# Performance work log

Measured on AMD Instinct MI355X. Metric: run time of the kernel, lower is better.

The kernel has to match this reference:

```python
import jax, jax.numpy as jnp
import numpy as np

NUM_CLASSES = 80


def _bce_logits(x, y):
    # numerically stable BCEWithLogits, elementwise
    return jnp.maximum(x, 0.0) - x * y + jnp.log1p(jnp.exp(-jnp.abs(x)))


def _iou_center(b1, b2):
    # boxes in (cx, cy, w, h) format, last dim = 4; returns IoU, last dim dropped
    b1x1 = b1[..., 0] - b1[..., 2] / 2
    b1y1 = b1[..., 1] - b1[..., 3] / 2
    b1x2 = b1[..., 0] + b1[..., 2] / 2
    b1y2 = b1[..., 1] + b1[..., 3] / 2
    b2x1 = b2[..., 0] - b2[..., 2] / 2
    b2y1 = b2[..., 1] - b2[..., 3] / 2
    b2x2 = b2[..., 0] + b2[..., 2] / 2
    b2y2 = b2[..., 1] + b2[..., 3] / 2
    iw = jnp.clip(jnp.minimum(b1x2, b2x2) - jnp.maximum(b1x1, b2x1), 0.0)
    ih = jnp.clip(jnp.minimum(b1y2, b2y2) - jnp.maximum(b1y1, b2y1), 0.0)
    inter = iw * ih
    union = (b1x2 - b1x1) * (b1y2 - b1y1) + (b2x2 - b2x1) * (b2y2 - b2y1) - inter
    return inter / (union + 1e-16)


def setup_inputs() -> dict:
    key = jax.random.key(0)
    kp, ko, kxy, kwh, kc, ka = jax.random.split(key, 6)
    B, A, S = 32, 3, 52
    predictions = jax.random.normal(kp, (B, A, S, S, 5 + NUM_CLASSES), dtype=jnp.float32)
    obj_flag = jax.random.bernoulli(ko, 0.3, (B, A, S, S, 1)).astype(jnp.float32)
    xy = jax.random.uniform(kxy, (B, A, S, S, 2), dtype=jnp.float32)
    wh = jax.random.uniform(kwh, (B, A, S, S, 2), minval=0.05, maxval=1.5, dtype=jnp.float32)
    cls = jax.random.randint(kc, (B, A, S, S, 1), 0, NUM_CLASSES).astype(jnp.float32)
    target = jnp.concatenate([obj_flag, xy, wh, cls], axis=-1)
    anchors = jax.random.uniform(ka, (3, 2), minval=0.1, maxval=1.0, dtype=jnp.float32)
    return {"predictions": predictions, "target": target, "anchors": anchors}


def reference(predictions, target, anchors):
    obj = (target[..., 0] == 1).astype(predictions.dtype)    # [B,3,S,S]
    noobj = (target[..., 0] == 0).astype(predictions.dtype)  # [B,3,S,S]
    n_obj = jnp.sum(obj)
    n_noobj = jnp.sum(noobj)

    anchors_r = anchors.reshape(1, 3, 1, 1, 2)
    pred_obj = predictions[..., 0]
    tgt_obj = target[..., 0]

    # noobj BCE (masked mean over noobj cells)
    no_detection = jnp.sum(_bce_logits(pred_obj, tgt_obj) * noobj) / n_noobj

    # decoded boxes and IoU (detached)
    pred_xy = jax.nn.sigmoid(predictions[..., 1:3])
    pred_wh_dec = jnp.exp(predictions[..., 3:5]) * anchors_r
    box_preds = jnp.concatenate([pred_xy, pred_wh_dec], axis=-1)
    ious = jax.lax.stop_gradient(_iou_center(box_preds, target[..., 1:5]))  # [B,3,S,S]

    # obj BCE against IoU-scaled targets (masked mean over obj cells)
    detection = jnp.sum(_bce_logits(pred_obj, ious * tgt_obj) * obj) / n_obj

    # box MSE: sigmoid(xy) & raw wh vs target xy & log(wh/anchors)
    pred_box = jnp.concatenate([pred_xy, predictions[..., 3:5]], axis=-1)
    tgt_box = jnp.concatenate(
        [target[..., 1:3], jnp.log(1e-16 + target[..., 3:5] / anchors_r)], axis=-1)
    box = jnp.sum(((pred_box - tgt_box) ** 2) * obj[..., None]) / (4.0 * n_obj)

    # classification CE (masked mean over obj cells)
    logp = jax.nn.log_softmax(predictions[..., 5:], axis=-1)
    labels = target[..., 5].astype(jnp.int32)
    nll = -jnp.take_along_axis(logp, labels[..., None], axis=-1)[..., 0]
    classification = jnp.sum(nll * obj) / n_obj

    return box + detection + no_detection + classification
```

## Files before the change

### kernel.cpp

```cpp
#include <hip/hip_runtime.h>

#define NTHREADS  256
#define STRIDE    85
#define SSPAN     2704
#define NEG_HUGE  -3.0e38f

__device__ __forceinline__ float wave_reduce(float v) {
    #pragma unroll
    for (int off = 32; off > 0; off >>= 1)
        v += __shfl_down(v, off, 64);
    return v;
}

__global__ __launch_bounds__(NTHREADS) void loss_partial(
    const float* __restrict__ pred, const float* __restrict__ tgt,
    const float* __restrict__ anchors, float* __restrict__ partial,
    int n_cells, int ngroups)
{
    __shared__ float red[4][6];

    const int tid  = threadIdx.x;
    const int lane = tid & 63;
    const int wid  = tid >> 6;

    const float aw0 = anchors[0], ah0 = anchors[1];
    const float aw1 = anchors[2], ah1 = anchors[3];
    const float aw2 = anchors[4], ah2 = anchors[5];

    float a_obj = 0.f, a_nobj = 0.f, a_bceo = 0.f, a_bceno = 0.f,
          a_box = 0.f, a_cls = 0.f;

    const int gstride = gridDim.x * 4;
    for (int g = blockIdx.x * 4 + wid; g < ngroups; g += gstride) {
        const int cbase = g * 64;
        const int cell  = cbase + lane;
        const bool valid = cell < n_cells;

        float t0 = -1.f, t1 = 0.f, t2 = 0.f, t3 = 0.f, t4 = 0.f, t5 = 0.f;
        float p0 = 0.f;
        if (valid) {
            const float* tc = tgt + (size_t)cell * 6;
            t0 = tc[0]; t1 = tc[1]; t2 = tc[2];
            t3 = tc[3]; t4 = tc[4]; t5 = tc[5];
            p0 = pred[(size_t)cell * STRIDE];
        }
        const float bce_base = fmaxf(p0, 0.f) + log1pf(__expf(-fabsf(p0)));
        if (t0 == 0.0f) { a_nobj += 1.f; a_bceno += bce_base; }
        if (t0 == 1.0f) { a_obj  += 1.f; }

        unsigned long long m = __ballot(t0 == 1.0f);

        int c0 = -1; float f1a = 0.f, f2a = 0.f;
        if (m) {
            c0 = __ffsll(m) - 1; m &= m - 1;
            const float* b = pred + (size_t)(cbase + c0) * STRIDE;
            f1a = b[1 + lane];
            if (lane < 20) f2a = b[65 + lane];
        }
        while (c0 >= 0) {
            int c1 = -1; float f1b = 0.f, f2b = 0.f;
            if (m) {
                c1 = __ffsll(m) - 1; m &= m - 1;
                const float* b = pred + (size_t)(cbase + c1) * STRIDE;
                f1b = b[1 + lane];
                if (lane < 20) f2b = b[65 + lane];
            }
            {
                const int cg = cbase + c0;
                const float m1 = (lane >= 4) ? f1a : NEG_HUGE;
                const float m2 = (lane < 20) ? f2a : NEG_HUGE;
                float mx = fmaxf(m1, m2);
                #pragma unroll
                for (int o = 32; o; o >>= 1) mx = fmaxf(mx, __shfl_xor(mx, o, 64));
                float e = ((lane >= 4) ? __expf(f1a - mx) : 0.f)
                        + ((lane < 20) ? __expf(f2a - mx) : 0.f);
                #pragma unroll
                for (int o = 32; o; o >>= 1) e += __shfl_xor(e, o, 64);

                const float tb1 = __shfl(t1, c0, 64), tb2 = __shfl(t2, c0, 64);
                const float tb3 = __shfl(t3, c0, 64), tb4 = __shfl(t4, c0, 64);
                const float tb5 = __shfl(t5, c0, 64);
                const float pb0 = __shfl(p0, c0, 64);
                const float bb  = __shfl(bce_base, c0, 64);
                const float pp1 = __shfl(f1a, 0, 64), pp2 = __shfl(f1a, 1, 64);
                const float pp3 = __shfl(f1a, 2, 64), pp4 = __shfl(f1a, 3, 64);

                const int   label = (int)tb5;
                const int   idx   = 5 + label;
                const float s1 = __shfl(f1a, (idx - 1) & 63, 64);
                const float s2 = __shfl(f2a, (idx - 65) & 63, 64);
                const float lv = (idx <= 64) ? s1 : s2;

                const int aidx = (cg / SSPAN) % 3;
                const float aw = aidx == 0 ? aw0 : (aidx == 1 ? aw1 : aw2);
                const float ah = aidx == 0 ? ah0 : (aidx == 1 ? ah1 : ah2);

                const float sx = 1.f / (1.f + __expf(-pp1));
                const float sy = 1.f / (1.f + __expf(-pp2));
                const float pw = __expf(pp3) * aw, ph = __expf(pp4) * ah;
                const float b1x1 = sx - pw * 0.5f, b1x2 = sx + pw * 0.5f;
                const float b1y1 = sy - ph * 0.5f, b1y2 = sy + ph * 0.5f;
                const float b2x1 = tb1 - tb3 * 0.5f, b2x2 = tb1 + tb3 * 0.5f;
                const float b2y1 = tb2 - tb4 * 0.5f, b2y2 = tb2 + tb4 * 0.5f;
                const float iw = fmaxf(fminf(b1x2, b2x2) - fmaxf(b1x1, b2x1), 0.f);
                const float ih = fmaxf(fminf(b1y2, b2y2) - fmaxf(b1y1, b2y1), 0.f);
                const float inter = iw * ih;
                const float uni = (b1x2 - b1x1) * (b1y2 - b1y1)
                                + (b2x2 - b2x1) * (b2y2 - b2y1) - inter;
                const float iou = inter / (uni + 1e-16f);

                const float vbceo = bb - pb0 * iou;
                const float lw = logf(1e-16f + tb3 / aw);
                const float lh = logf(1e-16f + tb4 / ah);
                const float d0 = sx - tb1, d1 = sy - tb2;
                const float d2 = pp3 - lw, d3 = pp4 - lh;
                const float vbox = d0 * d0 + d1 * d1 + d2 * d2 + d3 * d3;
                const float vcls = (mx + __logf(e)) - lv;

                if (lane == c0) {
                    a_bceo += vbceo;
                    a_box  += vbox;
                    a_cls  += vcls;
                }
            }
            c0 = c1; f1a = f1b; f2a = f2b;
        }
    }

    float vals[6] = {a_obj, a_nobj, a_bceo, a_bceno, a_box, a_cls};
    #pragma unroll
    for (int k = 0; k < 6; ++k) {
        const float r = wave_reduce(vals[k]);
        if (lane == 0) red[wid][k] = r;
    }
    __syncthreads();
    if (tid == 0) {
        #pragma unroll
        for (int k = 0; k < 6; ++k)
            partial[blockIdx.x * 6 + k] =
                red[0][k] + red[1][k] + red[2][k] + red[3][k];
    }
}

__global__ __launch_bounds__(NTHREADS) void loss_final(
    const float* __restrict__ partial, int nblocks, float* __restrict__ out)
{
    __shared__ float red[4][6];
    const int tid = threadIdx.x, lane = tid & 63, wid = tid >> 6;
    float s[6] = {0.f, 0.f, 0.f, 0.f, 0.f, 0.f};
    for (int i = tid; i < nblocks; i += NTHREADS) {
        #pragma unroll
        for (int k = 0; k < 6; ++k) s[k] += partial[i * 6 + k];
    }
    #pragma unroll
    for (int k = 0; k < 6; ++k) {
        const float r = wave_reduce(s[k]);
        if (lane == 0) red[wid][k] = r;
    }
    __syncthreads();
    if (tid == 0) {
        float t[6];
        #pragma unroll
        for (int k = 0; k < 6; ++k)
            t[k] = red[0][k] + red[1][k] + red[2][k] + red[3][k];
        const float n_obj = t[0], n_noobj = t[1];
        out[0] = t[2] / n_obj + t[3] / n_noobj
               + t[4] / (4.f * n_obj) + t[5] / n_obj;
    }
}

extern "C" void kernel_launch(void* const* d_in, const int* in_sizes, int n_in,
                              void* d_out, int out_size, void* d_ws, size_t ws_size,
                              hipStream_t stream) {
    const float* pred    = (const float*)d_in[0];
    const float* tgt     = (const float*)d_in[1];
    const float* anchors = (const float*)d_in[2];
    float* out = (float*)d_out;

    const int n_cells = in_sizes[1] / 6;
    const int ngroups = (n_cells + 63) / 64;
    int grid = (ngroups + 3) / 4;
    if (grid > 2048) grid = 2048;
    if (grid < 1)    grid = 1;
    float* partial = (float*)d_ws;

    loss_partial<<<grid, NTHREADS, 0, stream>>>(pred, tgt, anchors, partial,
                                                n_cells, ngroups);
    loss_final<<<1, NTHREADS, 0, stream>>>(partial, grid, out);
}
```

Baseline: 163.9 us.

## Compact object cells into shared queue and process four lanes per cell

Replaces the per-wave serial loop over object cells, where a whole 64-lane wave handled one cell at a time with wide shuffles, with a block-level compaction. Object cells in a 256-cell tile are written to a shared-memory queue, and each cell is then handled by 4 lanes that load 20 class logits apiece and reduce with 4-wide shuffles. The aim is to use far more of each wave per object cell and to drop the serial dependency chain. In exchange it adds __syncthreads barriers per tile and contiguous per-lane loads that are less coalesced. Target loads also switch to float2.

After: 135.9 us. 1.21x faster.

```diff
diff --git a/kernel.cpp b/kernel.cpp
--- a/kernel.cpp
+++ b/kernel.cpp
@@ -1,9 +1,10 @@
 #include <hip/hip_runtime.h>
 
 #define NTHREADS  256
+#define TILE      256
 #define STRIDE    85
 #define SSPAN     2704
-#define NEG_HUGE  -3.0e38f
+#define MAXGRID   2048
 
 __device__ __forceinline__ float wave_reduce(float v) {
     #pragma unroll
@@ -15,13 +16,19 @@
 __global__ __launch_bounds__(NTHREADS) void loss_partial(
     const float* __restrict__ pred, const float* __restrict__ tgt,
     const float* __restrict__ anchors, float* __restrict__ partial,
-    int n_cells, int ngroups)
+    int n_cells, int n_tiles)
 {
+    __shared__ int   qcell[TILE];
+    __shared__ int   qlab [TILE];
+    __shared__ float qt1[TILE], qt2[TILE], qt3[TILE], qt4[TILE];
+    __shared__ float qp0[TILE], qbb[TILE];
+    __shared__ int   wcnt[4];
     __shared__ float red[4][6];
 
     const int tid  = threadIdx.x;
     const int lane = tid & 63;
     const int wid  = tid >> 6;
+    const int part = tid & 3;
 
     const float aw0 = anchors[0], ah0 = anchors[1];
     const float aw1 = anchors[2], ah1 = anchors[3];
@@ -30,68 +37,74 @@
     float a_obj = 0.f, a_nobj = 0.f, a_bceo = 0.f, a_bceno = 0.f,
           a_box = 0.f, a_cls = 0.f;
 
-    const int gstride = gridDim.x * 4;
-    for (int g = blockIdx.x * 4 + wid; g < ngroups; g += gstride) {
-        const int cbase = g * 64;
-        const int cell  = cbase + lane;
+    for (int tile = blockIdx.x; tile < n_tiles; tile += gridDim.x) {
+        const int cell  = tile * TILE + tid;
         const bool valid = cell < n_cells;
 
         float t0 = -1.f, t1 = 0.f, t2 = 0.f, t3 = 0.f, t4 = 0.f, t5 = 0.f;
         float p0 = 0.f;
         if (valid) {
-            const float* tc = tgt + (size_t)cell * 6;
-            t0 = tc[0]; t1 = tc[1]; t2 = tc[2];
-            t3 = tc[3]; t4 = tc[4]; t5 = tc[5];
+            const float2* tc2 = (const float2*)(tgt + (size_t)cell * 6);
+            const float2 a = tc2[0], b = tc2[1], c = tc2[2];
+            t0 = a.x; t1 = a.y; t2 = b.x; t3 = b.y; t4 = c.x; t5 = c.y;
             p0 = pred[(size_t)cell * STRIDE];
         }
         const float bce_base = fmaxf(p0, 0.f) + log1pf(__expf(-fabsf(p0)));
         if (t0 == 0.0f) { a_nobj += 1.f; a_bceno += bce_base; }
-        if (t0 == 1.0f) { a_obj  += 1.f; }
+        const bool isobj = (t0 == 1.0f);
+        if (isobj) a_obj += 1.f;
 
-        unsigned long long m = __ballot(t0 == 1.0f);
+        const unsigned long long m = __ballot(isobj);
+        if (lane == 0) wcnt[wid] = __popcll(m);
+        __syncthreads();
+        int off = 0;
+        #pragma unroll
+        for (int w = 0; w < 4; ++w) if (w < wid) off += wcnt[w];
+        const int nq = wcnt[0] + wcnt[1] + wcnt[2] + wcnt[3];
+        if (isobj) {
+            const int rank = off + __popcll(m & ((1ull << lane) - 1ull));
+            qcell[rank] = cell;
+            qt1[rank] = t1; qt2[rank] = t2; qt3[rank] = t3; qt4[rank] = t4;
+            qlab[rank] = (int)t5;
+            qp0[rank]  = p0;
+            qbb[rank]  = bce_base;
+        }
+        __syncthreads();
 
-        int c0 = -1; float f1a = 0.f, f2a = 0.f;
-        if (m) {
-            c0 = __ffsll(m) - 1; m &= m - 1;
-            const float* b = pred + (size_t)(cbase + c0) * STRIDE;
-            f1a = b[1 + lane];
-            if (lane < 20) f2a = b[65 + lane];
-        }
-        while (c0 >= 0) {
-            int c1 = -1; float f1b = 0.f, f2b = 0.f;
-            if (m) {
-                c1 = __ffsll(m) - 1; m &= m - 1;
-                const float* b = pred + (size_t)(cbase + c1) * STRIDE;
-                f1b = b[1 + lane];
-                if (lane < 20) f2b = b[65 + lane];
-            }
-            {
-                const int cg = cbase + c0;
-                const float m1 = (lane >= 4) ? f1a : NEG_HUGE;
-                const float m2 = (lane < 20) ? f2a : NEG_HUGE;
-                float mx = fmaxf(m1, m2);
-                #pragma unroll
-                for (int o = 32; o; o >>= 1) mx = fmaxf(mx, __shfl_xor(mx, o, 64));
-                float e = ((lane >= 4) ? __expf(f1a - mx) : 0.f)
-                        + ((lane < 20) ? __expf(f2a - mx) : 0.f);
-                #pragma unroll
-                for (int o = 32; o; o >>= 1) e += __shfl_xor(e, o, 64);
+        const int nr = (nq + 63) >> 6;
+        for (int r = 0; r < nr; ++r) {
+            const int qi  = r * 64 + (tid >> 2);
+            const bool act = qi < nq;
+            const int cellg = act ? qcell[qi] : 0;
+            const float* pc = pred + (size_t)cellg * STRIDE;
 
-                const float tb1 = __shfl(t1, c0, 64), tb2 = __shfl(t2, c0, 64);
-                const float tb3 = __shfl(t3, c0, 64), tb4 = __shfl(t4, c0, 64);
-                const float tb5 = __shfl(t5, c0, 64);
-                const float pb0 = __shfl(p0, c0, 64);
-                const float bb  = __shfl(bce_base, c0, 64);
-                const float pp1 = __shfl(f1a, 0, 64), pp2 = __shfl(f1a, 1, 64);
-                const float pp3 = __shfl(f1a, 2, 64), pp4 = __shfl(f1a, 3, 64);
+            float v[20];
+            const float* cp = pc + 5 + part * 20;
+            #pragma unroll
+            for (int k = 0; k < 20; ++k) v[k] = cp[k];
+            float mx = v[0];
+            #pragma unroll
+            for (int k = 1; k < 20; ++k) mx = fmaxf(mx, v[k]);
+            mx = fmaxf(mx, __shfl_xor(mx, 1, 4));
+            mx = fmaxf(mx, __shfl_xor(mx, 2, 4));
+            float se = 0.f;
+            #pragma unroll
+            for (int k = 0; k < 20; ++k) se += __expf(v[k] - mx);
+            se += __shfl_xor(se, 1, 4);
+            se += __shfl_xor(se, 2, 4);
 
-                const int   label = (int)tb5;
-                const int   idx   = 5 + label;
-                const float s1 = __shfl(f1a, (idx - 1) & 63, 64);
-                const float s2 = __shfl(f2a, (idx - 65) & 63, 64);
-                const float lv = (idx <= 64) ? s1 : s2;
+            const float pp  = pc[1 + part];
+            const float pp1 = __shfl(pp, 0, 4), pp2 = __shfl(pp, 1, 4);
+            const float pp3 = __shfl(pp, 2, 4), pp4 = __shfl(pp, 3, 4);
 
-                const int aidx = (cg / SSPAN) % 3;
+            if (part == 0 && act) {
+                const float tb1 = qt1[qi], tb2 = qt2[qi];
+                const float tb3 = qt3[qi], tb4 = qt4[qi];
+                const int   label = qlab[qi];
+                const float pb0 = qp0[qi], bb = qbb[qi];
+                const float lv  = pc[5 + label];
+
+                const int aidx = (cellg / SSPAN) % 3;
                 const float aw = aidx == 0 ? aw0 : (aidx == 1 ? aw1 : aw2);
                 const float ah = aidx == 0 ? ah0 : (aidx == 1 ? ah1 : ah2);
 
@@ -109,22 +122,16 @@
                                 + (b2x2 - b2x1) * (b2y2 - b2y1) - inter;
                 const float iou = inter / (uni + 1e-16f);
 
-                const float vbceo = bb - pb0 * iou;
+                a_bceo += bb - pb0 * iou;
                 const float lw = logf(1e-16f + tb3 / aw);
                 const float lh = logf(1e-16f + tb4 / ah);
                 const float d0 = sx - tb1, d1 = sy - tb2;
                 const float d2 = pp3 - lw, d3 = pp4 - lh;
-                const float vbox = d0 * d0 + d1 * d1 + d2 * d2 + d3 * d3;
-                const float vcls = (mx + __logf(e)) - lv;
-
-                if (lane == c0) {
-                    a_bceo += vbceo;
-                    a_box  += vbox;
-                    a_cls  += vcls;
-                }
+                a_box += d0 * d0 + d1 * d1 + d2 * d2 + d3 * d3;
+                a_cls += (mx + __logf(se)) - lv;
             }
-            c0 = c1; f1a = f1b; f2a = f2b;
         }
+        __syncthreads();
     }
 
     float vals[6] = {a_obj, a_nobj, a_bceo, a_bceno, a_box, a_cls};
@@ -178,13 +185,12 @@
     float* out = (float*)d_out;
 
     const int n_cells = in_sizes[1] / 6;
-    const int ngroups = (n_cells + 63) / 64;
-    int grid = (ngroups + 3) / 4;
-    if (grid > 2048) grid = 2048;
-    if (grid < 1)    grid = 1;
+    const int n_tiles = (n_cells + TILE - 1) / TILE;
+    int grid = n_tiles < MAXGRID ? n_tiles : MAXGRID;
+    if (grid < 1) grid = 1;
     float* partial = (float*)d_ws;
 
     loss_partial<<<grid, NTHREADS, 0, stream>>>(pred, tgt, anchors, partial,
-                                                n_cells, ngroups);
+                                                n_cells, n_tiles);
     loss_final<<<1, NTHREADS, 0, stream>>>(partial, grid, out);
 }
```
